# Kernel optimization log

Measured on AMD Instinct MI355X. Metric: run time of the kernel, lower is better.

Reference implementation:

```python
import jax, jax.numpy as jnp
import numpy as np

B, N, C, H = 8, 4096, 768, 32
D = C // H  # head_dim = 24
EPS = 1e-12


def _l2norm(t):
    # F.normalize(dim=-1): t / max(||t||_2, eps)
    n = jnp.sqrt(jnp.sum(t * t, axis=-1, keepdims=True))
    return t / jnp.maximum(n, EPS)


def setup_inputs() -> dict:
    key = jax.random.key(0)
    ks = jax.random.split(key, 6)
    s_in = 1.0 / np.sqrt(C)
    return {
        "x": jax.random.normal(ks[0], (B, N, C), dtype=jnp.float32),
        "W_qkv": jax.random.uniform(ks[1], (C, 3 * C), jnp.float32, -s_in, s_in),
        "b_qkv": jax.random.uniform(ks[2], (3 * C,), jnp.float32, -s_in, s_in),
        "temperature": jnp.ones((H, 1, 1), dtype=jnp.float32),
        "W_proj": jax.random.uniform(ks[3], (C, C), jnp.float32, -s_in, s_in),
        "b_proj": jax.random.uniform(ks[4], (C,), jnp.float32, -s_in, s_in),
    }


def reference(x, W_qkv, b_qkv, temperature, W_proj, b_proj):
    b, n, c = x.shape
    qkv = x @ W_qkv + b_qkv                                  # (B,N,3C)
    qkv = qkv.reshape(b, n, 3, H, D).transpose(2, 0, 3, 1, 4)  # (3,B,H,N,D)
    q, k, v = qkv[0], qkv[1], qkv[2]                         # (B,H,N,D)
    q = jnp.swapaxes(q, -1, -2)                              # (B,H,D,N)
    k = jnp.swapaxes(k, -1, -2)
    v = jnp.swapaxes(v, -1, -2)
    q = _l2norm(q)                                           # normalize over N
    k = _l2norm(k)
    attn = jnp.einsum('bhdn,bhen->bhde', q, k) * temperature  # (B,H,D,D)
    attn = jax.nn.softmax(attn, axis=-1)
    y = jnp.einsum('bhde,bhen->bhdn', attn, v)               # (B,H,D,N)
    # Faithful to torch: (1,B,H,D,N).transpose(1,2).reshape(B,N,C)
    # == (H,B,D,N) flattened row-major into (B,N,C)
    y = jnp.transpose(y, (1, 0, 2, 3)).reshape(b, n, c)
    return y @ W_proj + b_proj
```

## Files before the change

### kernel.cpp

```cpp
#include <hip/hip_runtime.h>
#include <hip/hip_bf16.h>


#define DEVI __device__ __forceinline__

typedef __attribute__((ext_vector_type(8))) short bf16x8;
typedef __attribute__((ext_vector_type(4))) float f32x4;
typedef unsigned int u32;
typedef unsigned short u16;

DEVI u16 f2bf(float f) {
  union { float f; u32 u; } x; x.f = f;
  u32 r = x.u + 0x7FFFu + ((x.u >> 16) & 1u);
  return (u16)(r >> 16);
}

DEVI void gload_lds16(const void* g, void* l) {
  __builtin_amdgcn_global_load_lds((__attribute__((address_space(1))) void*)g,
                                   (__attribute__((address_space(3))) void*)l, 16, 0, 0);
}

__global__ __launch_bounds__(256) void cvt_kernel(const float* __restrict__ in,
                                                  u16* __restrict__ out, int n8) {
  int i = blockIdx.x * 256 + threadIdx.x;
  if (i >= n8) return;
  long o = (long)i * 8;
  float4 a = *(const float4*)(in + o);
  float4 b = *(const float4*)(in + o + 4);
  uint4 v;
  v.x = f2bf(a.x) | ((u32)f2bf(a.y) << 16);
  v.y = f2bf(a.z) | ((u32)f2bf(a.w) << 16);
  v.z = f2bf(b.x) | ((u32)f2bf(b.y) << 16);
  v.w = f2bf(b.z) | ((u32)f2bf(b.w) << 16);
  *(uint4*)(out + o) = v;
}

__global__ __launch_bounds__(256) void transpose_cvt(const float* __restrict__ W,
                                                     u16* __restrict__ Wt, int K, int N) {
  __shared__ float tile[32][33];
  int n0 = blockIdx.x * 32, k0 = blockIdx.y * 32;
  int tx = threadIdx.x, ty = threadIdx.y;
  #pragma unroll
  for (int i = 0; i < 4; ++i)
    tile[ty + 8 * i][tx] = W[(long)(k0 + ty + 8 * i) * N + n0 + tx];
  __syncthreads();
  #pragma unroll
  for (int i = 0; i < 4; ++i)
    Wt[(long)(n0 + ty + 8 * i) * K + k0 + tx] = f2bf(tile[tx][ty + 8 * i]);
}

template<int NT, int BF16_OUT>
__global__ __launch_bounds__(512, 4) void gemm2b_kernel(
    const u16* __restrict__ A, const u16* __restrict__ Bt,
    const float* __restrict__ bias, void* __restrict__ Cout,
    int M, int N) {
  constexpr int K = NT * 64;
  __shared__ __attribute__((aligned(128))) char lds[65536];

  int nbx = N >> 7;
  int nwg = gridDim.x;
  int bid = blockIdx.x;
  bid = (bid & 7) * (nwg >> 3) + (bid >> 3);
  int bx = bid % nbx, by = bid / nbx;

  int t = threadIdx.x;
  int w = t >> 6, l = t & 63;
  int wr = w >> 2, wc = w & 3;
  int l16 = l & 15, l4 = l >> 4;

  int cbb = (l4 * 16) ^ ((l16 & 8) << 2);
  int pA0 = (wr * 64 + l16) * 64 + cbb;
  int pB0 = 32768 + (wc * 32 + l16) * 64 + cbb;

  int pin = t * 16;
  int lam = pin ^ (((pin >> 9) & 1) << 5);
  int soff = (lam >> 6) * K + ((lam & 63) >> 1);

  const u16* Ag = A + (long)by * 128 * K;
  const u16* Bg = Bt + (long)bx * 128 * K;
  int sdA = w * 1024;

  f32x4 acc[4][2] = {};

  #pragma unroll
  for (int j = 0; j < 2; ++j) {
    gload_lds16(Ag + soff + j * 32, lds + j * 8192 + sdA);
    gload_lds16(Bg + soff + j * 32, lds + 32768 + j * 8192 + sdA);
  }

  for (int kt = 0; kt < NT; ++kt) {
    int s = kt & 1;
    if (kt + 1 < NT) {
      #pragma unroll
      for (int j = 0; j < 2; ++j) {
        gload_lds16(Ag + soff + (kt + 1) * 64 + j * 32,
                    lds + (s ^ 1) * 16384 + j * 8192 + sdA);
        gload_lds16(Bg + soff + (kt + 1) * 64 + j * 32,
                    lds + 32768 + (s ^ 1) * 16384 + j * 8192 + sdA);
      }
      asm volatile("s_waitcnt vmcnt(4)" ::: "memory");
    } else {
      asm volatile("s_waitcnt vmcnt(0)" ::: "memory");
    }
    __builtin_amdgcn_sched_barrier(0);
    __builtin_amdgcn_s_barrier();
    __builtin_amdgcn_sched_barrier(0);

    bf16x8 aF[4][2], bF[2][2];
    #pragma unroll
    for (int mi = 0; mi < 4; ++mi)
      #pragma unroll
      for (int ks = 0; ks < 2; ++ks)
        aF[mi][ks] = *(const bf16x8*)(lds + s * 16384 + ks * 8192 + mi * 1024 + pA0);
    #pragma unroll
    for (int n = 0; n < 2; ++n)
      #pragma unroll
      for (int ks = 0; ks < 2; ++ks)
        bF[n][ks] = *(const bf16x8*)(lds + s * 16384 + ks * 8192 + n * 1024 + pB0);

    __builtin_amdgcn_s_setprio(1);
    #pragma unroll
    for (int mi = 0; mi < 4; ++mi)
      #pragma unroll
      for (int n = 0; n < 2; ++n) {
        acc[mi][n] = __builtin_amdgcn_mfma_f32_16x16x32_bf16(aF[mi][0], bF[n][0], acc[mi][n], 0, 0, 0);
        acc[mi][n] = __builtin_amdgcn_mfma_f32_16x16x32_bf16(aF[mi][1], bF[n][1], acc[mi][n], 0, 0, 0);
      }
    __builtin_amdgcn_s_setprio(0);
    __builtin_amdgcn_s_barrier();
    __builtin_amdgcn_sched_barrier(0);
  }

  #pragma unroll
  for (int mi = 0; mi < 4; ++mi) {
    int row0 = by * 128 + wr * 64 + mi * 16 + l4 * 4;
    #pragma unroll
    for (int n = 0; n < 2; ++n) {
      int col = bx * 128 + wc * 32 + n * 16 + l16;
      float bv = bias[col];
      #pragma unroll
      for (int j = 0; j < 4; ++j) {
        long idx = (long)(row0 + j) * N + col;
        float v = acc[mi][n][j] + bv;
        if (BF16_OUT) ((u16*)Cout)[idx] = f2bf(v);
        else          ((float*)Cout)[idx] = v;
      }
    }
  }
}

__global__ __launch_bounds__(256) void attn_kernel(const u16* __restrict__ qkv,
                                                   const float* __restrict__ temperature,
                                                   u16* __restrict__ yout) {
  __shared__ u16 qt[32][136];
  __shared__ u16 kt[32][136];
  __shared__ u16 vl[128][40];
  __shared__ u16 attnb[32][40];
  __shared__ float Gs[32][33];
  __shared__ float sq[32];
  __shared__ float sk[32];

  int bid = blockIdx.x;
  int b = bid >> 5, h = bid & 31;
  int t = threadIdx.x;
  int w = t >> 6, l = t & 63;
  int l16 = l & 15, l4 = l >> 4;
  int fm = w >> 1, fn = w & 1;

  for (int i = t; i < 32 * 136; i += 256) { qt[0][i] = 0; kt[0][i] = 0; }
  for (int i = t; i < 128 * 40; i += 256) vl[0][i] = 0;
  for (int i = t; i < 32 * 40; i += 256) attnb[0][i] = 0;
  __syncthreads();

  f32x4 accG = {}, accQ = {}, accK = {};
  const u16* qbase = qkv + (long)b * 4096 * 2304 + h * 24;

  for (int nc = 0; nc < 32; ++nc) {
    int n0 = nc * 128;
    #pragma unroll
    for (int i = 0; i < 6; ++i) {
      int idx = t + 256 * i;
      int n = idx / 12, dw = idx % 12;
      const u16* p = qbase + (long)(n0 + n) * 2304 + dw * 2;
      u32 uq = *(const u32*)p;
      u32 uk = *(const u32*)(p + 768);
      qt[dw * 2][n] = (u16)uq; qt[dw * 2 + 1][n] = (u16)(uq >> 16);
      kt[dw * 2][n] = (u16)uk; kt[dw * 2 + 1][n] = (u16)(uk >> 16);
    }
    __syncthreads();
    #pragma unroll
    for (int ks = 0; ks < 4; ++ks) {
      int koff = ks * 32 + l4 * 8;
      bf16x8 qa = *(const bf16x8*)&qt[fm * 16 + l16][koff];
      bf16x8 qb = *(const bf16x8*)&qt[fn * 16 + l16][koff];
      bf16x8 ka = *(const bf16x8*)&kt[fm * 16 + l16][koff];
      bf16x8 kb = *(const bf16x8*)&kt[fn * 16 + l16][koff];
      accG = __builtin_amdgcn_mfma_f32_16x16x32_bf16(qa, kb, accG, 0, 0, 0);
      accQ = __builtin_amdgcn_mfma_f32_16x16x32_bf16(qa, qb, accQ, 0, 0, 0);
      accK = __builtin_amdgcn_mfma_f32_16x16x32_bf16(ka, kb, accK, 0, 0, 0);
    }
    __syncthreads();
  }

  #pragma unroll
  for (int j = 0; j < 4; ++j) Gs[fm * 16 + l4 * 4 + j][fn * 16 + l16] = accG[j];
  if (fm == fn) {
    #pragma unroll
    for (int j = 0; j < 4; ++j)
      if (l4 * 4 + j == l16) { sq[fm * 16 + l16] = accQ[j]; sk[fm * 16 + l16] = accK[j]; }
  }
  __syncthreads();

  if (t < 24) {
    float nq = fmaxf(sqrtf(fmaxf(sq[t], 0.f)), 1e-12f);
    float tmp = temperature[h];
    float p[24]; float mx = -1e30f;
    #pragma unroll
    for (int e = 0; e < 24; ++e) {
      float nk = fmaxf(sqrtf(fmaxf(sk[e], 0.f)), 1e-12f);
      float a = Gs[t][e] / (nq * nk) * tmp;
      p[e] = a; mx = fmaxf(mx, a);
    }
    float s = 0.f;
    #pragma unroll
    for (int e = 0; e < 24; ++e) { p[e] = __expf(p[e] - mx); s += p[e]; }
    float inv = 1.f / s;
    #pragma unroll
    for (int e = 0; e < 24; ++e) attnb[t][e] = f2bf(p[e] * inv);
  }
  __syncthreads();

  bf16x8 af0 = *(const bf16x8*)&attnb[l16][l4 * 8];
  bf16x8 af1 = *(const bf16x8*)&attnb[16 + l16][l4 * 8];
  const u16* vbase = qbase + 1536;
  u16* ybase = yout + (long)(h * 8 + b) * 24 * 4096;

  for (int nc = 0; nc < 32; ++nc) {
    int n0 = nc * 128;
    #pragma unroll
    for (int i = 0; i < 6; ++i) {
      int idx = t + 256 * i;
      int n = idx / 12, dw = idx % 12;
      u32 uv = *(const u32*)(vbase + (long)(n0 + n) * 2304 + dw * 2);
      *(u32*)&vl[n][dw * 2] = uv;
    }
    __syncthreads();
    f32x4 z = {};
    #pragma unroll
    for (int fnn = 0; fnn < 2; ++fnn) {
      int ncol = w * 32 + fnn * 16 + l16;
      bf16x8 bv = *(const bf16x8*)&vl[ncol][l4 * 8];
      f32x4 y0 = __builtin_amdgcn_mfma_f32_16x16x32_bf16(af0, bv, z, 0, 0, 0);
      f32x4 y1 = __builtin_amdgcn_mfma_f32_16x16x32_bf16(af1, bv, z, 0, 0, 0);
      int gn = n0 + ncol;
      #pragma unroll
      for (int j = 0; j < 4; ++j) {
        int d0 = l4 * 4 + j;
        ybase[(long)d0 * 4096 + gn] = f2bf(y0[j]);
        int d1 = 16 + d0;
        if (d1 < 24) ybase[(long)d1 * 4096 + gn] = f2bf(y1[j]);
      }
    }
    __syncthreads();
  }
}

extern "C" void kernel_launch(void* const* d_in, const int* in_sizes, int n_in,
                              void* d_out, int out_size, void* d_ws, size_t ws_size,
                              hipStream_t stream) {
  const float* x     = (const float*)d_in[0];
  const float* Wqkv  = (const float*)d_in[1];
  const float* bqkv  = (const float*)d_in[2];
  const float* temp  = (const float*)d_in[3];
  const float* Wproj = (const float*)d_in[4];
  const float* bproj = (const float*)d_in[5];
  float* out = (float*)d_out;

  char* ws = (char*)d_ws;
  u16* xb  = (u16*)(ws);
  u16* wqt = (u16*)(ws + 50331648);
  u16* wpt = (u16*)(ws + 53870592);
  u16* qkv = (u16*)(ws + 55050240);
  u16* y   = xb;

  cvt_kernel<<<12288, 256, 0, stream>>>(x, xb, 3145728);
  transpose_cvt<<<dim3(72, 24), dim3(32, 8), 0, stream>>>(Wqkv, wqt, 768, 2304);
  transpose_cvt<<<dim3(24, 24), dim3(32, 8), 0, stream>>>(Wproj, wpt, 768, 768);
  gemm2b_kernel<12, 1><<<4608, 512, 0, stream>>>(xb, wqt, bqkv, qkv, 32768, 2304);
  attn_kernel<<<256, 256, 0, stream>>>(qkv, temp, y);
  gemm2b_kernel<12, 0><<<1536, 512, 0, stream>>>(y, wpt, bproj, out, 32768, 768);
}
```

Before: 314.1 us.

## Widen GEMM tile to 128x256, prefetch attention loads into registers

The GEMM moves from 128x128 tiles with K-step 64 to 128x256 tiles with K-step 32. Each wave now holds a 64x64 accumulator, which doubles B reuse per A fragment and halves the workgroup count. GEMM outputs are written with nontemporal stores. The attention kernel now double-buffers its global q/k and v loads in registers, fetching two chunks ahead, to hide global latency behind the MFMA work. The trade-offs are more accumulator registers, which may lower occupancy, and more K-loop iterations, each with its own barriers.

```diff
diff --git a/kernel.cpp b/kernel.cpp
--- a/kernel.cpp
+++ b/kernel.cpp
@@ -54,10 +54,10 @@
     const u16* __restrict__ A, const u16* __restrict__ Bt,
     const float* __restrict__ bias, void* __restrict__ Cout,
     int M, int N) {
-  constexpr int K = NT * 64;
-  __shared__ __attribute__((aligned(128))) char lds[65536];
-
-  int nbx = N >> 7;
+  constexpr int K = NT * 32;
+  __shared__ __attribute__((aligned(128))) char lds[49152];
+
+  int nbx = N >> 8;
   int nwg = gridDim.x;
   int bid = blockIdx.x;
   bid = (bid & 7) * (nwg >> 3) + (bid >> 3);
@@ -70,35 +70,39 @@
 
   int cbb = (l4 * 16) ^ ((l16 & 8) << 2);
   int pA0 = (wr * 64 + l16) * 64 + cbb;
-  int pB0 = 32768 + (wc * 32 + l16) * 64 + cbb;
-
-  int pin = t * 16;
-  int lam = pin ^ (((pin >> 9) & 1) << 5);
-  int soff = (lam >> 6) * K + ((lam & 63) >> 1);
+  int pB0 = 16384 + (wc * 64 + l16) * 64 + cbb;
+
+  int pa = t * 16;
+  int la = pa ^ (((pa >> 9) & 1) << 5);
+  int soffA = (la >> 6) * K + ((la & 63) >> 1);
+  int soffB[2];
+  #pragma unroll
+  for (int j = 0; j < 2; ++j) {
+    int p = (j * 512 + t) * 16;
+    int lb = p ^ (((p >> 9) & 1) << 5);
+    soffB[j] = (lb >> 6) * K + ((lb & 63) >> 1);
+  }
 
   const u16* Ag = A + (long)by * 128 * K;
-  const u16* Bg = Bt + (long)bx * 128 * K;
-  int sdA = w * 1024;
-
-  f32x4 acc[4][2] = {};
-
-  #pragma unroll
-  for (int j = 0; j < 2; ++j) {
-    gload_lds16(Ag + soff + j * 32, lds + j * 8192 + sdA);
-    gload_lds16(Bg + soff + j * 32, lds + 32768 + j * 8192 + sdA);
-  }
+  const u16* Bg = Bt + (long)bx * 256 * K;
+  int sdst = w * 1024;
+
+  f32x4 acc[4][4] = {};
+
+  gload_lds16(Ag + soffA, lds + sdst);
+  #pragma unroll
+  for (int j = 0; j < 2; ++j)
+    gload_lds16(Bg + soffB[j], lds + 16384 + j * 8192 + sdst);
 
   for (int kt = 0; kt < NT; ++kt) {
     int s = kt & 1;
     if (kt + 1 < NT) {
+      gload_lds16(Ag + soffA + (kt + 1) * 32, lds + (s ^ 1) * 8192 + sdst);
       #pragma unroll
-      for (int j = 0; j < 2; ++j) {
-        gload_lds16(Ag + soff + (kt + 1) * 64 + j * 32,
-                    lds + (s ^ 1) * 16384 + j * 8192 + sdA);
-        gload_lds16(Bg + soff + (kt + 1) * 64 + j * 32,
-                    lds + 32768 + (s ^ 1) * 16384 + j * 8192 + sdA);
-      }
-      asm volatile("s_waitcnt vmcnt(4)" ::: "memory");
+      for (int j = 0; j < 2; ++j)
+        gload_lds16(Bg + soffB[j] + (kt + 1) * 32,
+                    lds + 16384 + (s ^ 1) * 16384 + j * 8192 + sdst);
+      asm volatile("s_waitcnt vmcnt(3)" ::: "memory");
     } else {
       asm volatile("s_waitcnt vmcnt(0)" ::: "memory");
     }
@@ -106,26 +110,20 @@
     __builtin_amdgcn_s_barrier();
     __builtin_amdgcn_sched_barrier(0);
 
-    bf16x8 aF[4][2], bF[2][2];
+    bf16x8 aF[4], bF[4];
+    #pragma unroll
+    for (int mi = 0; mi < 4; ++mi)
+      aF[mi] = *(const bf16x8*)(lds + s * 8192 + mi * 1024 + pA0);
+    #pragma unroll
+    for (int n = 0; n < 4; ++n)
+      bF[n] = *(const bf16x8*)(lds + s * 16384 + n * 1024 + pB0);
+
+    __builtin_amdgcn_s_setprio(1);
     #pragma unroll
     for (int mi = 0; mi < 4; ++mi)
       #pragma unroll
-      for (int ks = 0; ks < 2; ++ks)
-        aF[mi][ks] = *(const bf16x8*)(lds + s * 16384 + ks * 8192 + mi * 1024 + pA0);
-    #pragma unroll
-    for (int n = 0; n < 2; ++n)
-      #pragma unroll
-      for (int ks = 0; ks < 2; ++ks)
-        bF[n][ks] = *(const bf16x8*)(lds + s * 16384 + ks * 8192 + n * 1024 + pB0);
-
-    __builtin_amdgcn_s_setprio(1);
-    #pragma unroll
-    for (int mi = 0; mi < 4; ++mi)
-      #pragma unroll
-      for (int n = 0; n < 2; ++n) {
-        acc[mi][n] = __builtin_amdgcn_mfma_f32_16x16x32_bf16(aF[mi][0], bF[n][0], acc[mi][n], 0, 0, 0);
-        acc[mi][n] = __builtin_amdgcn_mfma_f32_16x16x32_bf16(aF[mi][1], bF[n][1], acc[mi][n], 0, 0, 0);
-      }
+      for (int n = 0; n < 4; ++n)
+        acc[mi][n] = __builtin_amdgcn_mfma_f32_16x16x32_bf16(aF[mi], bF[n], acc[mi][n], 0, 0, 0);
     __builtin_amdgcn_s_setprio(0);
     __builtin_amdgcn_s_barrier();
     __builtin_amdgcn_sched_barrier(0);
@@ -135,19 +133,67 @@
   for (int mi = 0; mi < 4; ++mi) {
     int row0 = by * 128 + wr * 64 + mi * 16 + l4 * 4;
     #pragma unroll
-    for (int n = 0; n < 2; ++n) {
-      int col = bx * 128 + wc * 32 + n * 16 + l16;
+    for (int n = 0; n < 4; ++n) {
+      int col = bx * 256 + wc * 64 + n * 16 + l16;
       float bv = bias[col];
       #pragma unroll
       for (int j = 0; j < 4; ++j) {
         long idx = (long)(row0 + j) * N + col;
         float v = acc[mi][n][j] + bv;
-        if (BF16_OUT) ((u16*)Cout)[idx] = f2bf(v);
-        else          ((float*)Cout)[idx] = v;
+        if (BF16_OUT) __builtin_nontemporal_store(f2bf(v), (u16*)Cout + idx);
+        else          __builtin_nontemporal_store(v, (float*)Cout + idx);
       }
     }
   }
 }
+
+#define PFQK(nc, rq, rk)                                                       \
+  { long cb = (long)(nc) * 294912;                                             \
+    _Pragma("unroll") for (int i = 0; i < 6; ++i) {                            \
+      rq[i] = *(const u32*)(qbase + cb + offi[i]);                             \
+      rk[i] = *(const u32*)(qbase + cb + offi[i] + 768); } }
+
+#define WRQK(rq, rk)                                                           \
+  { _Pragma("unroll") for (int i = 0; i < 6; ++i) {                            \
+      qt[dv[i] * 2][nv[i]] = (u16)rq[i];                                       \
+      qt[dv[i] * 2 + 1][nv[i]] = (u16)(rq[i] >> 16);                           \
+      kt[dv[i] * 2][nv[i]] = (u16)rk[i];                                       \
+      kt[dv[i] * 2 + 1][nv[i]] = (u16)(rk[i] >> 16); } }
+
+#define GRAM_MFMA                                                              \
+  { _Pragma("unroll") for (int ks = 0; ks < 4; ++ks) {                         \
+      int koff = ks * 32 + l4 * 8;                                             \
+      bf16x8 qa = *(const bf16x8*)&qt[fm * 16 + l16][koff];                    \
+      bf16x8 qb = *(const bf16x8*)&qt[fn * 16 + l16][koff];                    \
+      bf16x8 ka = *(const bf16x8*)&kt[fm * 16 + l16][koff];                    \
+      bf16x8 kb = *(const bf16x8*)&kt[fn * 16 + l16][koff];                    \
+      accG = __builtin_amdgcn_mfma_f32_16x16x32_bf16(qa, kb, accG, 0, 0, 0);   \
+      accQ = __builtin_amdgcn_mfma_f32_16x16x32_bf16(qa, qb, accQ, 0, 0, 0);   \
+      accK = __builtin_amdgcn_mfma_f32_16x16x32_bf16(ka, kb, accK, 0, 0, 0); } }
+
+#define PFV(nc, rv)                                                            \
+  { long cb = (long)(nc) * 294912;                                             \
+    _Pragma("unroll") for (int i = 0; i < 6; ++i)                              \
+      rv[i] = *(const u32*)(vbase + cb + offi[i]); }
+
+#define WRV(rv)                                                                \
+  { _Pragma("unroll") for (int i = 0; i < 6; ++i)                              \
+      *(u32*)&vl[nv[i]][dv[i] * 2] = rv[i]; }
+
+#define PV_STORE(nc)                                                           \
+  { int n0 = (nc) * 128;                                                       \
+    f32x4 z = {};                                                              \
+    _Pragma("unroll") for (int fnn = 0; fnn < 2; ++fnn) {                      \
+      int ncol = w * 32 + fnn * 16 + l16;                                      \
+      bf16x8 bv = *(const bf16x8*)&vl[ncol][l4 * 8];                           \
+      f32x4 y0 = __builtin_amdgcn_mfma_f32_16x16x32_bf16(af0, bv, z, 0, 0, 0); \
+      f32x4 y1 = __builtin_amdgcn_mfma_f32_16x16x32_bf16(af1, bv, z, 0, 0, 0); \
+      int gn = n0 + ncol;                                                      \
+      _Pragma("unroll") for (int j = 0; j < 4; ++j) {                          \
+        int d0 = l4 * 4 + j;                                                   \
+        ybase[(long)d0 * 4096 + gn] = f2bf(y0[j]);                             \
+        int d1 = 16 + d0;                                                      \
+        if (d1 < 24) ybase[(long)d1 * 4096 + gn] = f2bf(y1[j]); } } }
 
 __global__ __launch_bounds__(256) void attn_kernel(const u16* __restrict__ qkv,
                                                    const float* __restrict__ temperature,
@@ -170,35 +216,34 @@
   for (int i = t; i < 32 * 136; i += 256) { qt[0][i] = 0; kt[0][i] = 0; }
   for (int i = t; i < 128 * 40; i += 256) vl[0][i] = 0;
   for (int i = t; i < 32 * 40; i += 256) attnb[0][i] = 0;
-  __syncthreads();
+
+  int nv[6], dv[6], offi[6];
+  #pragma unroll
+  for (int i = 0; i < 6; ++i) {
+    int idx = t + 256 * i;
+    nv[i] = idx / 12; dv[i] = idx % 12;
+    offi[i] = nv[i] * 2304 + dv[i] * 2;
+  }
 
   f32x4 accG = {}, accQ = {}, accK = {};
   const u16* qbase = qkv + (long)b * 4096 * 2304 + h * 24;
-
-  for (int nc = 0; nc < 32; ++nc) {
-    int n0 = nc * 128;
-    #pragma unroll
-    for (int i = 0; i < 6; ++i) {
-      int idx = t + 256 * i;
-      int n = idx / 12, dw = idx % 12;
-      const u16* p = qbase + (long)(n0 + n) * 2304 + dw * 2;
-      u32 uq = *(const u32*)p;
-      u32 uk = *(const u32*)(p + 768);
-      qt[dw * 2][n] = (u16)uq; qt[dw * 2 + 1][n] = (u16)(uq >> 16);
-      kt[dw * 2][n] = (u16)uk; kt[dw * 2 + 1][n] = (u16)(uk >> 16);
-    }
-    __syncthreads();
-    #pragma unroll
-    for (int ks = 0; ks < 4; ++ks) {
-      int koff = ks * 32 + l4 * 8;
-      bf16x8 qa = *(const bf16x8*)&qt[fm * 16 + l16][koff];
-      bf16x8 qb = *(const bf16x8*)&qt[fn * 16 + l16][koff];
-      bf16x8 ka = *(const bf16x8*)&kt[fm * 16 + l16][koff];
-      bf16x8 kb = *(const bf16x8*)&kt[fn * 16 + l16][koff];
-      accG = __builtin_amdgcn_mfma_f32_16x16x32_bf16(qa, kb, accG, 0, 0, 0);
-      accQ = __builtin_amdgcn_mfma_f32_16x16x32_bf16(qa, qb, accQ, 0, 0, 0);
-      accK = __builtin_amdgcn_mfma_f32_16x16x32_bf16(ka, kb, accK, 0, 0, 0);
-    }
+  const u16* vbase = qbase + 1536;
+
+  u32 rqA[6], rkA[6], rqB[6], rkB[6];
+  PFQK(0, rqA, rkA);
+  PFQK(1, rqB, rkB);
+  __syncthreads();
+
+  for (int nc = 0; nc < 32; nc += 2) {
+    WRQK(rqA, rkA);
+    __syncthreads();
+    if (nc + 2 < 32) PFQK(nc + 2, rqA, rkA);
+    GRAM_MFMA;
+    __syncthreads();
+    WRQK(rqB, rkB);
+    __syncthreads();
+    if (nc + 3 < 32) PFQK(nc + 3, rqB, rkB);
+    GRAM_MFMA;
     __syncthreads();
   }
 
@@ -228,39 +273,26 @@
     #pragma unroll
     for (int e = 0; e < 24; ++e) attnb[t][e] = f2bf(p[e] * inv);
   }
+
+  u32 rvA[6], rvB[6];
+  PFV(0, rvA);
+  PFV(1, rvB);
   __syncthreads();
 
   bf16x8 af0 = *(const bf16x8*)&attnb[l16][l4 * 8];
   bf16x8 af1 = *(const bf16x8*)&attnb[16 + l16][l4 * 8];
-  const u16* vbase = qbase + 1536;
   u16* ybase = yout + (long)(h * 8 + b) * 24 * 4096;
 
-  for (int nc = 0; nc < 32; ++nc) {
-    int n0 = nc * 128;
-    #pragma unroll
-    for (int i = 0; i < 6; ++i) {
-      int idx = t + 256 * i;
-      int n = idx / 12, dw = idx % 12;
-      u32 uv = *(const u32*)(vbase + (long)(n0 + n) * 2304 + dw * 2);
-      *(u32*)&vl[n][dw * 2] = uv;
-    }
-    __syncthreads();
-    f32x4 z = {};
-    #pragma unroll
-    for (int fnn = 0; fnn < 2; ++fnn) {
-      int ncol = w * 32 + fnn * 16 + l16;
-      bf16x8 bv = *(const bf16x8*)&vl[ncol][l4 * 8];
-      f32x4 y0 = __builtin_amdgcn_mfma_f32_16x16x32_bf16(af0, bv, z, 0, 0, 0);
-      f32x4 y1 = __builtin_amdgcn_mfma_f32_16x16x32_bf16(af1, bv, z, 0, 0, 0);
-      int gn = n0 + ncol;
-      #pragma unroll
-      for (int j = 0; j < 4; ++j) {
-        int d0 = l4 * 4 + j;
-        ybase[(long)d0 * 4096 + gn] = f2bf(y0[j]);
-        int d1 = 16 + d0;
-        if (d1 < 24) ybase[(long)d1 * 4096 + gn] = f2bf(y1[j]);
-      }
-    }
+  for (int nc = 0; nc < 32; nc += 2) {
+    WRV(rvA);
+    __syncthreads();
+    if (nc + 2 < 32) PFV(nc + 2, rvA);
+    PV_STORE(nc);
+    __syncthreads();
+    WRV(rvB);
+    __syncthreads();
+    if (nc + 3 < 32) PFV(nc + 3, rvB);
+    PV_STORE(nc + 1);
     __syncthreads();
   }
 }
@@ -286,7 +318,7 @@
   cvt_kernel<<<12288, 256, 0, stream>>>(x, xb, 3145728);
   transpose_cvt<<<dim3(72, 24), dim3(32, 8), 0, stream>>>(Wqkv, wqt, 768, 2304);
   transpose_cvt<<<dim3(24, 24), dim3(32, 8), 0, stream>>>(Wproj, wpt, 768, 768);
-  gemm2b_kernel<12, 1><<<4608, 512, 0, stream>>>(xb, wqt, bqkv, qkv, 32768, 2304);
+  gemm2b_kernel<24, 1><<<2304, 512, 0, stream>>>(xb, wqt, bqkv, qkv, 32768, 2304);
   attn_kernel<<<256, 256, 0, stream>>>(qkv, temp, y);
-  gemm2b_kernel<12, 0><<<1536, 512, 0, stream>>>(y, wpt, bproj, out, 32768, 768);
-}
+  gemm2b_kernel<24, 0><<<768, 512, 0, stream>>>(y, wpt, bproj, out, 32768, 768);
+}
```

Result: no change. 320.1 us (+1.9%).
